# Performance work log

Hardware: AMD Instinct MI355X
Metric: run time of the kernel (lower is better)

The kernel has to match this reference:

```python
import jax, jax.numpy as jnp
import numpy as np

N_NODES = 10000
NUM_FEAT = 128
HIDD = 256
HEADS = 8
NUM_CLASS = 10
NEG_SLOPE = 0.2


def _gat_conv(x, src, dst, W, att_src, att_dst, bias, n_nodes):
    # x: [N, F_in]; W: [F_in, H*C]; att_*: [H, C]; bias: [H*C]
    H, C = att_src.shape
    h = (x @ W).reshape(n_nodes, H, C)                      # [N, H, C]
    a_src = jnp.einsum('nhc,hc->nh', h, att_src)            # [N, H]
    a_dst = jnp.einsum('nhc,hc->nh', h, att_dst)            # [N, H]
    e = a_src[src] + a_dst[dst]                             # [E, H]
    e = jnp.where(e >= 0, e, NEG_SLOPE * e)                 # leaky_relu
    # segment softmax over edges grouped by destination node
    e_max = jax.ops.segment_max(jax.lax.stop_gradient(e), dst, num_segments=n_nodes)
    e_max = jnp.where(jnp.isfinite(e_max), e_max, 0.0)
    ex = jnp.exp(e - e_max[dst])                            # [E, H]
    denom = jax.ops.segment_sum(ex, dst, num_segments=n_nodes)
    alpha = ex / (denom[dst] + 1e-16)                       # [E, H]
    msg = h[src] * alpha[:, :, None]                        # [E, H, C]
    out = jax.ops.segment_sum(msg, dst, num_segments=n_nodes)
    return out.reshape(n_nodes, H * C) + bias


def setup_inputs() -> dict:
    key = jax.random.key(0)
    ks = jax.random.split(key, 12)
    x = jax.random.normal(ks[0], (N_NODES, NUM_FEAT), dtype=jnp.float32)
    edge_index = jax.random.randint(ks[1], (2, 50000), 0, N_NODES, dtype=jnp.int64)
    g1 = 1.0 / np.sqrt(NUM_FEAT)
    g2 = 1.0 / np.sqrt(HEADS * HIDD)
    return {
        'x': x,
        'edge_index': edge_index,
        'W1': jax.random.normal(ks[2], (NUM_FEAT, HEADS * HIDD), dtype=jnp.float32) * g1,
        'att_src1': jax.random.normal(ks[3], (HEADS, HIDD), dtype=jnp.float32) * g2,
        'att_dst1': jax.random.normal(ks[4], (HEADS, HIDD), dtype=jnp.float32) * g2,
        'b1': jnp.zeros((HEADS * HIDD,), dtype=jnp.float32),
        'W2': jax.random.normal(ks[5], (HEADS * HIDD, NUM_CLASS), dtype=jnp.float32) * g2,
        'att_src2': jax.random.normal(ks[6], (1, NUM_CLASS), dtype=jnp.float32),
        'att_dst2': jax.random.normal(ks[7], (1, NUM_CLASS), dtype=jnp.float32),
        'b2': jnp.zeros((NUM_CLASS,), dtype=jnp.float32),
    }


def reference(x, edge_index, W1, att_src1, att_dst1, b1, W2, att_src2, att_dst2, b2):
    n = x.shape[0]
    # PyG GATConv default add_self_loops=True
    loop = jnp.arange(n, dtype=edge_index.dtype)
    src = jnp.concatenate([edge_index[0], loop])
    dst = jnp.concatenate([edge_index[1], loop])
    h = _gat_conv(x, src, dst, W1, att_src1, att_dst1, b1, n)
    h = jax.nn.elu(h)
    h = _gat_conv(h, src, dst, W2, att_src2, att_dst2, b2, n)
    return jax.nn.sigmoid(h)
```

## Files before the change

kernel.cpp:

```cpp
#include <hip/hip_runtime.h>
#include <math.h>

#define N_NODES 10000
#define N_PAD   10112
#define E0      50000
#define E_TOT   60000
#define FIN     128
#define HEADS   8
#define CHN     256
#define HC      2048
#define NC      10
#define NEG     0.2f
#define MAXD    128
#define MAXD2   64
#define LDSTR   80

typedef __attribute__((ext_vector_type(8))) short bf16x8;
typedef __attribute__((ext_vector_type(4))) float f32x4;

__device__ __forceinline__ unsigned f2u(float f){
  unsigned u = __float_as_uint(f);
  return (u & 0x80000000u) ? ~u : (u | 0x80000000u);
}
__device__ __forceinline__ float u2f(unsigned u){
  return __uint_as_float((u & 0x80000000u) ? (u & 0x7fffffffu) : ~u);
}
__device__ __forceinline__ unsigned short bf16_rne(float f){
  unsigned u = __float_as_uint(f);
  return (unsigned short)((u + 0x7FFFu + ((u >> 16) & 1u)) >> 16);
}

__global__ void k_init(const int* __restrict__ raw, int* __restrict__ flag,
                       int* __restrict__ deg, int* __restrict__ cursor){
  int t = blockIdx.x*256 + threadIdx.x;
  if (t < N_NODES){ deg[t] = 0; cursor[t] = 0; }
  if (blockIdx.x == 0 && threadIdx.x < 64){
    int i = threadIdx.x;
    bool bad = (raw[2*i + 1] != 0) || ((unsigned)raw[2*i] >= (unsigned)N_NODES);
    unsigned long long b = __ballot(bad);
    if (i == 0) *flag = (b == 0ull) ? 1 : 0;
  }
}

__global__ void k_convert(const int* __restrict__ raw, const int* __restrict__ flag,
                          int* __restrict__ esrc, int* __restrict__ edst,
                          int* __restrict__ deg){
  int e = blockIdx.x * blockDim.x + threadIdx.x;
  if (e >= E_TOT) return;
  int s, d;
  if (e < E0){
    if (*flag){ s = raw[2*e]; d = raw[2*(E0 + e)]; }
    else      { s = raw[e];   d = raw[E0 + e];     }
  } else {
    s = d = e - E0;
  }
  esrc[e] = s; edst[e] = d;
  atomicAdd(&deg[d], 1);
}

__global__ __launch_bounds__(256) void k_prepw(const float* __restrict__ W1,
                                               const float* __restrict__ att_src,
                                               const float* __restrict__ att_dst,
                                               unsigned short* __restrict__ w1t_hi,
                                               unsigned short* __restrict__ w1t_lo,
                                               float* __restrict__ vv){
  int t = blockIdx.x*256 + threadIdx.x;
  {
    int k = t >> 11;
    int n = t & 2047;
    float v = W1[(size_t)k*HC + n];
    unsigned short hi = bf16_rne(v);
    float hf = __uint_as_float((unsigned)hi << 16);
    unsigned short lo = bf16_rne(v - hf);
    w1t_hi[(size_t)n*FIN + k] = hi;
    w1t_lo[(size_t)n*FIN + k] = lo;
  }
  if (t < FIN*HEADS){
    int k = t >> 3, h = t & 7;
    const float* wrow = W1 + (size_t)k*HC + h*CHN;
    const float* as   = att_src + h*CHN;
    const float* ad   = att_dst + h*CHN;
    float s = 0.f, d = 0.f;
    #pragma unroll 4
    for (int c = 0; c < CHN; c += 4){
      float4 w = *reinterpret_cast<const float4*>(wrow + c);
      float4 a = *reinterpret_cast<const float4*>(as + c);
      float4 b = *reinterpret_cast<const float4*>(ad + c);
      s += w.x*a.x + w.y*a.y + w.z*a.z + w.w*a.w;
      d += w.x*b.x + w.y*b.y + w.z*b.z + w.w*b.w;
    }
    vv[k*16 + h]     = s;
    vv[k*16 + 8 + h] = d;
  }
}

__global__ __launch_bounds__(256) void k_attdot(const float* __restrict__ x,
                                                const float* __restrict__ vv,
                                                float* __restrict__ a_src,
                                                float* __restrict__ a_dst){
  const int wave = threadIdx.x >> 6, lane = threadIdx.x & 63;
  const int n = blockIdx.x*4 + wave;
  const int u = lane & 15, c = lane >> 4;
  const float* xr = x + (size_t)n*FIN + c*32;
  float acc = 0.f;
  #pragma unroll
  for (int q = 0; q < 8; ++q){
    float4 xv = *reinterpret_cast<const float4*>(xr + q*4);
    int k = c*32 + q*4;
    acc = fmaf(xv.x, vv[(k+0)*16 + u], acc);
    acc = fmaf(xv.y, vv[(k+1)*16 + u], acc);
    acc = fmaf(xv.z, vv[(k+2)*16 + u], acc);
    acc = fmaf(xv.w, vv[(k+3)*16 + u], acc);
  }
  acc += __shfl_xor(acc, 16);
  acc += __shfl_xor(acc, 32);
  if (c == 0){
    if (u < 8) a_src[n*HEADS + u] = acc;
    else       a_dst[n*HEADS + (u - 8)] = acc;
  }
}

__global__ __launch_bounds__(1024) void k_scan(const int* __restrict__ deg,
                                               int* __restrict__ offs){
  __shared__ int sums[1024];
  const int tid = threadIdx.x;
  int base = tid*10;
  int vals[10];
  int local = 0;
  #pragma unroll
  for (int i = 0; i < 10; ++i){
    int idx = base + i;
    int v = (idx < N_NODES) ? deg[idx] : 0;
    vals[i] = local;
    local += v;
  }
  sums[tid] = local;
  __syncthreads();
  for (int o = 1; o < 1024; o <<= 1){
    int t = (tid >= o) ? sums[tid - o] : 0;
    __syncthreads();
    sums[tid] += t;
    __syncthreads();
  }
  int boff = (tid == 0) ? 0 : sums[tid - 1];
  #pragma unroll
  for (int i = 0; i < 10; ++i){
    int idx = base + i;
    if (idx < N_NODES) offs[idx] = boff + vals[i];
  }
  if (tid == 1023) offs[N_NODES] = sums[1023];
}

__global__ void k_scatter(const int* __restrict__ esrc, const int* __restrict__ edst,
                          const int* __restrict__ offs, int* __restrict__ cursor,
                          int* __restrict__ csr_src){
  int e = blockIdx.x*256 + threadIdx.x;
  if (e < E_TOT){
    int d = edst[e];
    int pos = offs[d] + atomicAdd(&cursor[d], 1);
    csr_src[pos] = esrc[e];
  }
}

__global__ __launch_bounds__(128) void k_aggx(const float* __restrict__ x,
                                              const float* __restrict__ a_src1,
                                              const float* __restrict__ a_dst1,
                                              const int* __restrict__ offs,
                                              const int* __restrict__ csr_src,
                                              unsigned short* __restrict__ agg_hi,
                                              unsigned short* __restrict__ agg_lo){
  __shared__ float s_e[MAXD][HEADS];
  __shared__ int s_src[MAXD];
  __shared__ unsigned s_maxu[HEADS];
  __shared__ float s_sum[HEADS];
  __shared__ float s_inv[HEADS];
  __shared__ float s_ad[HEADS];
  const int n = blockIdx.x, tid = threadIdx.x;
  const int start = offs[n];
  int deg = offs[n+1] - start;
  if (deg > MAXD) deg = MAXD;
  if (tid < HEADS){
    s_maxu[tid] = 0u;
    s_sum[tid] = 0.f;
    s_ad[tid] = a_dst1[n*HEADS + tid];
  }
  for (int i = tid; i < deg; i += 128) s_src[i] = csr_src[start + i];
  __syncthreads();
  const int tot = deg*HEADS;
  for (int i = tid; i < tot; i += 128){
    int e = i >> 3, hh = i & 7;
    float v = a_src1[s_src[e]*HEADS + hh] + s_ad[hh];
    v = (v >= 0.f) ? v : NEG*v;
    s_e[e][hh] = v;
    atomicMax(&s_maxu[hh], f2u(v));
  }
  __syncthreads();
  for (int i = tid; i < tot; i += 128){
    int e = i >> 3, hh = i & 7;
    float v = expf(s_e[e][hh] - u2f(s_maxu[hh]));
    s_e[e][hh] = v;
    atomicAdd(&s_sum[hh], v);
  }
  __syncthreads();
  if (tid < HEADS) s_inv[tid] = 1.f/(s_sum[tid] + 1e-16f);
  __syncthreads();
  for (int i = tid; i < tot; i += 128) s_e[i>>3][i&7] *= s_inv[i&7];
  __syncthreads();
  float acc[HEADS] = {0,0,0,0,0,0,0,0};
  for (int e = 0; e < deg; ++e){
    float xv = x[(size_t)s_src[e]*FIN + tid];
    #pragma unroll
    for (int h = 0; h < HEADS; ++h) acc[h] = fmaf(s_e[e][h], xv, acc[h]);
  }
  #pragma unroll
  for (int h = 0; h < HEADS; ++h){
    float v = acc[h];
    unsigned short hi = bf16_rne(v);
    float hf = __uint_as_float((unsigned)hi << 16);
    unsigned short lo = bf16_rne(v - hf);
    size_t idx = ((size_t)h*N_PAD + n)*FIN + tid;
    agg_hi[idx] = hi;
    agg_lo[idx] = lo;
  }
}

__global__ __launch_bounds__(256, 4) void k_gemm1(const unsigned short* __restrict__ agg_hi,
                                                  const unsigned short* __restrict__ agg_lo,
                                                  const unsigned short* __restrict__ w1t_hi,
                                                  const unsigned short* __restrict__ w1t_lo,
                                                  const float* __restrict__ b1,
                                                  float* __restrict__ out1){
  __shared__ unsigned short Ahi[128*LDSTR];
  __shared__ unsigned short Alo[128*LDSTR];
  const int tid = threadIdx.x;
  const int bx = blockIdx.x;
  const int by = blockIdx.y;
  const int h  = bx >> 1;
  const int colbase = bx*128;
  const int n0 = by*128;
  const int wave = tid >> 6, lane = tid & 63;
  const int wr = wave >> 1, wc = wave & 1;
  const int nl = lane & 15, g = lane >> 4;
  const int colb = colbase + wc*64;

  const size_t plane = (size_t)h*N_PAD*FIN;

  f32x4 zero4 = {0.f, 0.f, 0.f, 0.f};
  f32x4 acc[4][4];
  #pragma unroll
  for (int fm = 0; fm < 4; ++fm)
    #pragma unroll
    for (int fn = 0; fn < 4; ++fn) acc[fm][fn] = zero4;

  #pragma unroll
  for (int ch = 0; ch < 2; ++ch){
    if (ch) __syncthreads();
    #pragma unroll
    for (int i = 0; i < 4; ++i){
      int cid = tid + 256*i;
      int row = cid >> 3, part = cid & 7;
      size_t gsrc = plane + (size_t)(n0 + row)*FIN + ch*64 + part*8;
      int ldst = row*LDSTR + part*8;
      *reinterpret_cast<bf16x8*>(&Ahi[ldst]) = *reinterpret_cast<const bf16x8*>(agg_hi + gsrc);
      *reinterpret_cast<bf16x8*>(&Alo[ldst]) = *reinterpret_cast<const bf16x8*>(agg_lo + gsrc);
    }
    __syncthreads();
    #pragma unroll
    for (int s = 0; s < 2; ++s){
      bf16x8 ah[4], al[4];
      #pragma unroll
      for (int fm = 0; fm < 4; ++fm){
        int lsrc = (wr*64 + fm*16 + nl)*LDSTR + s*32 + g*8;
        ah[fm] = *reinterpret_cast<const bf16x8*>(&Ahi[lsrc]);
        al[fm] = *reinterpret_cast<const bf16x8*>(&Alo[lsrc]);
      }
      #pragma unroll
      for (int fn = 0; fn < 4; ++fn){
        size_t bo = ((size_t)(colb + fn*16 + nl))*FIN + ch*64 + s*32 + g*8;
        bf16x8 bh = *reinterpret_cast<const bf16x8*>(w1t_hi + bo);
        bf16x8 bl = *reinterpret_cast<const bf16x8*>(w1t_lo + bo);
        #pragma unroll
        for (int fm = 0; fm < 4; ++fm){
          acc[fm][fn] = __builtin_amdgcn_mfma_f32_16x16x32_bf16(ah[fm], bh, acc[fm][fn], 0, 0, 0);
          acc[fm][fn] = __builtin_amdgcn_mfma_f32_16x16x32_bf16(ah[fm], bl, acc[fm][fn], 0, 0, 0);
          acc[fm][fn] = __builtin_amdgcn_mfma_f32_16x16x32_bf16(al[fm], bh, acc[fm][fn], 0, 0, 0);
        }
      }
    }
  }

  #pragma unroll
  for (int fm = 0; fm < 4; ++fm){
    #pragma unroll
    for (int fn = 0; fn < 4; ++fn){
      int col = colb + fn*16 + nl;
      float bb = b1[col];
      #pragma unroll
      for (int r = 0; r < 4; ++r){
        int row = n0 + wr*64 + fm*16 + g*4 + r;
        if (row < N_NODES){
          float v = acc[fm][fn][r] + bb;
          v = (v > 0.f) ? v : (__expf(v) - 1.f);
          out1[(size_t)row*HC + col] = v;
        }
      }
    }
  }
}

__global__ __launch_bounds__(256) void k_gemv2(const float* __restrict__ out1,
                                               const float* __restrict__ W2,
                                               const float* __restrict__ as2,
                                               const float* __restrict__ ad2,
                                               float* __restrict__ h2,
                                               float* __restrict__ a_src2,
                                               float* __restrict__ a_dst2){
  __shared__ float W2s[256][13];
  const int tid = threadIdx.x;
  const int nl = tid & 15;
  const int ng = tid >> 4;
  const int n = blockIdx.x*16 + ng;
  float acc[NC];
  #pragma unroll
  for (int j = 0; j < NC; ++j) acc[j] = 0.f;
  const float* row = out1 + (size_t)n*HC;
  for (int c = 0; c < 8; ++c){
    if (c) __syncthreads();
    {
      const float2* src = reinterpret_cast<const float2*>(W2 + (size_t)(c*256 + tid)*NC);
      #pragma unroll
      for (int q = 0; q < 5; ++q){
        float2 w = src[q];
        W2s[tid][2*q]   = w.x;
        W2s[tid][2*q+1] = w.y;
      }
    }
    __syncthreads();
    #pragma unroll
    for (int i = 0; i < 4; ++i){
      int kq = i*64 + nl*4;
      float4 v = *reinterpret_cast<const float4*>(row + c*256 + kq);
      float vm[4] = {v.x, v.y, v.z, v.w};
      #pragma unroll
      for (int m = 0; m < 4; ++m){
        const float* wrow = &W2s[kq + m][0];
        #pragma unroll
        for (int j = 0; j < NC; ++j)
          acc[j] = fmaf(vm[m], wrow[j], acc[j]);
      }
    }
  }
  #pragma unroll
  for (int o = 1; o < 16; o <<= 1){
    #pragma unroll
    for (int j = 0; j < NC; ++j) acc[j] += __shfl_xor(acc[j], o);
  }
  if (nl == 0){
    float ds = 0.f, dd = 0.f;
    #pragma unroll
    for (int j = 0; j < NC; ++j){
      h2[(size_t)n*NC + j] = acc[j];
      ds = fmaf(acc[j], as2[j], ds);
      dd = fmaf(acc[j], ad2[j], dd);
    }
    a_src2[n] = ds;
    a_dst2[n] = dd;
  }
}

__global__ __launch_bounds__(64) void k_agg2(const float* __restrict__ h2,
                                             const float* __restrict__ a_src2,
                                             const float* __restrict__ a_dst2,
                                             const int* __restrict__ offs,
                                             const int* __restrict__ csr_src,
                                             const float* __restrict__ b2,
                                             float* __restrict__ out){
  __shared__ float s_al[MAXD2];
  __shared__ int s_sc[MAXD2];
  const int n = blockIdx.x, lane = threadIdx.x;
  const int start = offs[n];
  int deg = offs[n+1] - start;
  if (deg > MAXD2) deg = MAXD2;
  const float ad = a_dst2[n];
  float e = -INFINITY;
  if (lane < deg){
    int src = csr_src[start + lane];
    s_sc[lane] = src;
    e = a_src2[src] + ad;
    e = (e >= 0.f) ? e : NEG*e;
  }
  float m = e;
  #pragma unroll
  for (int o = 1; o < 64; o <<= 1) m = fmaxf(m, __shfl_xor(m, o));
  float ex = (lane < deg) ? expf(e - m) : 0.f;
  float s = ex;
  #pragma unroll
  for (int o = 1; o < 64; o <<= 1) s += __shfl_xor(s, o);
  if (lane < deg) s_al[lane] = ex / (s + 1e-16f);
  __syncthreads();
  if (lane < NC){
    float acc = 0.f;
    for (int i = 0; i < deg; ++i)
      acc = fmaf(s_al[i], h2[(size_t)s_sc[i]*NC + lane], acc);
    float v = acc + b2[lane];
    out[n*NC + lane] = 1.f/(1.f + expf(-v));
  }
}

extern "C" void kernel_launch(void* const* d_in, const int* in_sizes, int n_in,
                              void* d_out, int out_size, void* d_ws, size_t ws_size,
                              hipStream_t stream){
  const float* x   = (const float*)d_in[0];
  const int*   ei  = (const int*)  d_in[1];
  const float* W1  = (const float*)d_in[2];
  const float* as1 = (const float*)d_in[3];
  const float* ad1 = (const float*)d_in[4];
  const float* b1  = (const float*)d_in[5];
  const float* W2  = (const float*)d_in[6];
  const float* as2 = (const float*)d_in[7];
  const float* ad2 = (const float*)d_in[8];
  const float* b2  = (const float*)d_in[9];
  float* out = (float*)d_out;

  char* ws = (char*)d_ws;
  size_t off = 0;
  auto alloc = [&](size_t bytes) -> void* {
    void* p = ws + off;
    off += (bytes + 255) & ~(size_t)255;
    return p;
  };
  float* out1    = (float*)alloc((size_t)N_NODES*HC*4);
  unsigned short* agg_hi = (unsigned short*)alloc((size_t)HEADS*N_PAD*FIN*2);
  unsigned short* agg_lo = (unsigned short*)alloc((size_t)HEADS*N_PAD*FIN*2);
  unsigned short* w1t_hi = (unsigned short*)alloc((size_t)HC*FIN*2);
  unsigned short* w1t_lo = (unsigned short*)alloc((size_t)HC*FIN*2);
  float* vv      = (float*)alloc((size_t)FIN*16*4);
  float* a_src1  = (float*)alloc((size_t)N_NODES*HEADS*4);
  float* a_dst1  = (float*)alloc((size_t)N_NODES*HEADS*4);
  float* h2      = (float*)alloc((size_t)N_NODES*NC*4);
  float* a_src2  = (float*)alloc((size_t)N_NODES*4);
  float* a_dst2  = (float*)alloc((size_t)N_NODES*4);
  int*   deg     = (int*)alloc((size_t)N_NODES*4);
  int*   offs    = (int*)alloc((size_t)(N_NODES+1)*4);
  int*   cursor  = (int*)alloc((size_t)N_NODES*4);
  int*   esrc    = (int*)alloc((size_t)E_TOT*4);
  int*   edst    = (int*)alloc((size_t)E_TOT*4);
  int*   csr_src = (int*)alloc((size_t)E_TOT*4);
  int*   flag    = (int*)alloc(4);
  (void)ws_size; (void)in_sizes; (void)n_in; (void)out_size;

  k_init   <<<40, 256, 0, stream>>>(ei, flag, deg, cursor);
  k_convert<<<(E_TOT + 255)/256, 256, 0, stream>>>(ei, flag, esrc, edst, deg);
  k_prepw  <<<(HC*FIN)/256, 256, 0, stream>>>(W1, as1, ad1, w1t_hi, w1t_lo, vv);
  k_attdot <<<N_NODES/4, 256, 0, stream>>>(x, vv, a_src1, a_dst1);
  k_scan   <<<1, 1024, 0, stream>>>(deg, offs);
  k_scatter<<<(E_TOT + 255)/256, 256, 0, stream>>>(esrc, edst, offs, cursor, csr_src);
  k_aggx   <<<N_NODES, 128, 0, stream>>>(x, a_src1, a_dst1, offs, csr_src, agg_hi, agg_lo);
  k_gemm1  <<<dim3(16, N_PAD/128), 256, 0, stream>>>(agg_hi, agg_lo, w1t_hi, w1t_lo, b1, out1);
  k_gemv2  <<<N_NODES/16, 256, 0, stream>>>(out1, W2, as2, ad2, h2, a_src2, a_dst2);
  k_agg2   <<<N_NODES, 64, 0, stream>>>(h2, a_src2, a_dst2, offs, csr_src, b2, out);
}
```

Measured before the change: 244.4 us.

## Pre-tile GEMM operands into MFMA fragment layout and drop LDS staging

The aggregation kernel and weight-prep kernel now write the bf16 hi/lo operands in a blocked 16-row by 8-element fragment order that matches the MFMA lane mapping. The GEMM then loads A and B fragments straight from global memory with contiguous 16-byte-per-lane loads, which removes the LDS tile, its stores and the barriers. This avoids shared-memory staging and sync overhead and may allow higher occupancy without the LDS footprint, but A tiles are no longer shared through LDS and rely on cache for reuse across waves. The launch-bounds occupancy hint was also dropped.

```diff
diff --git a/kernel.cpp b/kernel.cpp
--- a/kernel.cpp
+++ b/kernel.cpp
@@ -3,6 +3,7 @@
 
 #define N_NODES 10000
 #define N_PAD   10112
+#define NPB     632
 #define E0      50000
 #define E_TOT   60000
 #define FIN     128
@@ -13,10 +14,10 @@
 #define NEG     0.2f
 #define MAXD    128
 #define MAXD2   64
-#define LDSTR   80
 
 typedef __attribute__((ext_vector_type(8))) short bf16x8;
 typedef __attribute__((ext_vector_type(4))) float f32x4;
+
 
 __device__ __forceinline__ unsigned f2u(float f){
   unsigned u = __float_as_uint(f);
@@ -72,8 +73,10 @@
     unsigned short hi = bf16_rne(v);
     float hf = __uint_as_float((unsigned)hi << 16);
     unsigned short lo = bf16_rne(v - hf);
-    w1t_hi[(size_t)n*FIN + k] = hi;
-    w1t_lo[(size_t)n*FIN + k] = lo;
+    int cb = n >> 4, c = n & 15, klin = k >> 3, j = k & 7;
+    size_t idx = (size_t)cb*2048 + klin*128 + c*8 + j;
+    w1t_hi[idx] = hi;
+    w1t_lo[idx] = lo;
   }
   if (t < FIN*HEADS){
     int k = t >> 3, h = t & 7;
@@ -212,38 +215,35 @@
     #pragma unroll
     for (int h = 0; h < HEADS; ++h) acc[h] = fmaf(s_e[e][h], xv, acc[h]);
   }
+  const int rb = n >> 4, r = n & 15;
+  const int koff = (tid >> 3)*128 + r*8 + (tid & 7);
   #pragma unroll
   for (int h = 0; h < HEADS; ++h){
     float v = acc[h];
     unsigned short hi = bf16_rne(v);
     float hf = __uint_as_float((unsigned)hi << 16);
     unsigned short lo = bf16_rne(v - hf);
-    size_t idx = ((size_t)h*N_PAD + n)*FIN + tid;
+    size_t idx = ((size_t)h*NPB + rb)*2048 + koff;
     agg_hi[idx] = hi;
     agg_lo[idx] = lo;
   }
 }
 
-__global__ __launch_bounds__(256, 4) void k_gemm1(const unsigned short* __restrict__ agg_hi,
-                                                  const unsigned short* __restrict__ agg_lo,
-                                                  const unsigned short* __restrict__ w1t_hi,
-                                                  const unsigned short* __restrict__ w1t_lo,
-                                                  const float* __restrict__ b1,
-                                                  float* __restrict__ out1){
-  __shared__ unsigned short Ahi[128*LDSTR];
-  __shared__ unsigned short Alo[128*LDSTR];
+__global__ __launch_bounds__(256) void k_gemm1(const unsigned short* __restrict__ agg_hi,
+                                               const unsigned short* __restrict__ agg_lo,
+                                               const unsigned short* __restrict__ w1t_hi,
+                                               const unsigned short* __restrict__ w1t_lo,
+                                               const float* __restrict__ b1,
+                                               float* __restrict__ out1){
   const int tid = threadIdx.x;
   const int bx = blockIdx.x;
   const int by = blockIdx.y;
   const int h  = bx >> 1;
-  const int colbase = bx*128;
-  const int n0 = by*128;
   const int wave = tid >> 6, lane = tid & 63;
   const int wr = wave >> 1, wc = wave & 1;
   const int nl = lane & 15, g = lane >> 4;
-  const int colb = colbase + wc*64;
-
-  const size_t plane = (size_t)h*N_PAD*FIN;
+  const int colb = bx*128 + wc*64;
+  const int lelem = lane*8;
 
   f32x4 zero4 = {0.f, 0.f, 0.f, 0.f};
   f32x4 acc[4][4];
@@ -252,31 +252,24 @@
     #pragma unroll
     for (int fn = 0; fn < 4; ++fn) acc[fm][fn] = zero4;
 
+  const size_t arb0 = (size_t)h*NPB + by*8 + wr*4;
+  const size_t brb0 = (size_t)bx*8 + wc*4;
+
   #pragma unroll
   for (int ch = 0; ch < 2; ++ch){
-    if (ch) __syncthreads();
-    #pragma unroll
-    for (int i = 0; i < 4; ++i){
-      int cid = tid + 256*i;
-      int row = cid >> 3, part = cid & 7;
-      size_t gsrc = plane + (size_t)(n0 + row)*FIN + ch*64 + part*8;
-      int ldst = row*LDSTR + part*8;
-      *reinterpret_cast<bf16x8*>(&Ahi[ldst]) = *reinterpret_cast<const bf16x8*>(agg_hi + gsrc);
-      *reinterpret_cast<bf16x8*>(&Alo[ldst]) = *reinterpret_cast<const bf16x8*>(agg_lo + gsrc);
-    }
-    __syncthreads();
     #pragma unroll
     for (int s = 0; s < 2; ++s){
+      const int koff = (ch*8 + s*4)*128 + lelem;
       bf16x8 ah[4], al[4];
       #pragma unroll
       for (int fm = 0; fm < 4; ++fm){
-        int lsrc = (wr*64 + fm*16 + nl)*LDSTR + s*32 + g*8;
-        ah[fm] = *reinterpret_cast<const bf16x8*>(&Ahi[lsrc]);
-        al[fm] = *reinterpret_cast<const bf16x8*>(&Alo[lsrc]);
+        size_t ao = (arb0 + fm)*2048 + koff;
+        ah[fm] = *reinterpret_cast<const bf16x8*>(agg_hi + ao);
+        al[fm] = *reinterpret_cast<const bf16x8*>(agg_lo + ao);
       }
       #pragma unroll
       for (int fn = 0; fn < 4; ++fn){
-        size_t bo = ((size_t)(colb + fn*16 + nl))*FIN + ch*64 + s*32 + g*8;
+        size_t bo = (brb0 + fn)*2048 + koff;
         bf16x8 bh = *reinterpret_cast<const bf16x8*>(w1t_hi + bo);
         bf16x8 bl = *reinterpret_cast<const bf16x8*>(w1t_lo + bo);
         #pragma unroll
@@ -297,7 +290,7 @@
       float bb = b1[col];
       #pragma unroll
       for (int r = 0; r < 4; ++r){
-        int row = n0 + wr*64 + fm*16 + g*4 + r;
+        int row = by*128 + wr*64 + fm*16 + g*4 + r;
         if (row < N_NODES){
           float v = acc[fm][fn][r] + bb;
           v = (v > 0.f) ? v : (__expf(v) - 1.f);
```

Measured after the change: 239.6 us. No clear change (-2.0%).
